# Performance work log

Hardware: AMD Instinct MI355X
Metric: run time of the kernel (lower is better)

Reference implementation:

```python
import jax, jax.numpy as jnp
import numpy as np

B, S, D, H = 2, 2048, 2048, 16
HD = D // H            # 128
HALF = HD // 2         # 64
SOFTCAP = 50.0
ROPE_BASE = 10000.0


def setup_inputs() -> dict:
    key = jax.random.key(0)
    k1, k2, k3 = jax.random.split(key, 3)
    inputs = jax.random.normal(k1, (B, S, D), dtype=jnp.float32)
    # param init ~ nnx.initializers.normal() (stddev 0.01 default; scale to keep activations sane)
    w_in = jax.random.normal(k2, (D, H, 3 * HD), dtype=jnp.float32) * (1.0 / np.sqrt(D))
    w_out = jax.random.normal(k3, (H, HD, D), dtype=jnp.float32) * (1.0 / np.sqrt(D))
    # RoPE tables: [S, HALF]
    pos = jnp.arange(S, dtype=jnp.float32)[:, None]
    inv_freq = 1.0 / (ROPE_BASE ** (jnp.arange(HALF, dtype=jnp.float32) / HALF))
    ang = pos * inv_freq[None, :]
    rope_sin = jnp.sin(ang)
    rope_cos = jnp.cos(ang)
    # causal mask [1, 1, S, S]
    mask = jnp.tril(jnp.ones((S, S), dtype=bool))[None, None, :, :]
    return {"inputs": inputs, "w_in": w_in, "w_out": w_out,
            "rope_sin": rope_sin, "rope_cos": rope_cos, "mask": mask}


def apply_rope(x, sin, cos):
    # x: [B, S, H, HD]; sin/cos: [S, HALF] -> broadcast [1, S, 1, HALF]
    sin = sin[None, :, None, :]
    cos = cos[None, :, None, :]
    x1, x2 = x[..., :HALF], x[..., HALF:]
    return jnp.concatenate([x1 * cos - x2 * sin, x2 * cos + x1 * sin], axis=-1)


def reference(inputs, w_in, w_out, rope_sin, rope_cos, mask):
    dtype = inputs.dtype
    # fused QKV projection: [B, S, H, 3*HD]
    qkv = jnp.einsum('bsd,bhf->bshf'.replace('bhf', 'dhf'), inputs, w_in)
    q, k, v = jnp.split(qkv, 3, axis=-1)           # each [B, S, H, HD]
    q = apply_rope(q, rope_sin, rope_cos)
    k = apply_rope(k, rope_sin, rope_cos)
    q = q / jnp.sqrt(jnp.asarray(HD, dtype))
    scores = jnp.einsum('bqhd,bkhd->bhqk', q, k)   # [B, H, S, S]
    big_neg = jnp.finfo(dtype).min
    scores = jnp.where(mask, scores, big_neg)
    scores = jnp.tanh(scores / SOFTCAP) * SOFTCAP  # softcap
    attn = jax.nn.softmax(scores, axis=-1)
    x = jnp.einsum('bhqk,bkhd->bqhd', attn, v)     # [B, S, H, HD]
    out = jnp.einsum('bqhd,hdm->bqm', x, w_out)    # [B, S, D]
    return out
```

## Files before the change

kernel.cpp:

```cpp
#include <hip/hip_runtime.h>

#define B_ 2
#define S_ 2048
#define D_ 2048
#define H_ 16
#define HD_ 128
#define NT_ (S_ / 64)
#define NBUF 6

typedef unsigned short u16;
typedef __bf16 bf16x8 __attribute__((ext_vector_type(8)));
typedef float f32x4 __attribute__((ext_vector_type(4)));

__device__ __forceinline__ float bf2f(u16 u) {
  unsigned int x = ((unsigned int)u) << 16;
  return __builtin_bit_cast(float, x);
}
__device__ __forceinline__ u16 f2bf(float f) {
  unsigned int u = __builtin_bit_cast(unsigned int, f);
  u += 0x7fffu + ((u >> 16) & 1u);
  return (u16)(u >> 16);
}
__device__ __forceinline__ void async16(const void* g, void* l) {
  __builtin_amdgcn_global_load_lds((const __attribute__((address_space(1))) void*)g,
                                   (__attribute__((address_space(3))) void*)l, 16, 0, 0);
}
__device__ __forceinline__ float vexp2(float x) {
  float r;
  asm("v_exp_f32 %0, %1" : "=v"(r) : "v"(x));
  return r;
}
__device__ __forceinline__ float vrcp(float x) {
  float r;
  asm("v_rcp_f32 %0, %1" : "=v"(r) : "v"(x));
  return r;
}

__global__ __launch_bounds__(256) void conv_f32_bf16(const float* __restrict__ in,
                                                     u16* __restrict__ outp, int n) {
  int idx = (blockIdx.x * 256 + threadIdx.x) * 4;
  int stride = gridDim.x * 256 * 4;
  for (; idx < n; idx += stride) {
    float4 v = *(const float4*)(in + idx);
    ushort4 ov = make_ushort4(f2bf(v.x), f2bf(v.y), f2bf(v.z), f2bf(v.w));
    *(ushort4*)(outp + idx) = ov;
  }
}

__global__ __launch_bounds__(256) void transpose_conv(const float* __restrict__ in,
                                                      u16* __restrict__ outp, int R, int C) {
  __shared__ float tile[32][33];
  int c0 = blockIdx.x * 32, r0 = blockIdx.y * 32;
  int tx = threadIdx.x & 31, ty = threadIdx.x >> 5;
#pragma unroll
  for (int yy = 0; yy < 32; yy += 8)
    tile[ty + yy][tx] = in[(size_t)(r0 + ty + yy) * C + c0 + tx];
  __syncthreads();
#pragma unroll
  for (int yy = 0; yy < 32; yy += 8)
    outp[(size_t)(c0 + ty + yy) * R + r0 + tx] = f2bf(tile[tx][ty + yy]);
}

__global__ __launch_bounds__(256) void transpose_v(const u16* __restrict__ in,
                                                   u16* __restrict__ outp) {
  __shared__ u16 tile[32][33];
  int bhh = blockIdx.z;
  const u16* ip = in + (size_t)bhh * S_ * HD_;
  u16* op = outp + (size_t)bhh * HD_ * S_;
  int hd0 = blockIdx.x * 32, s0 = blockIdx.y * 32;
  int tx = threadIdx.x & 31, ty = threadIdx.x >> 5;
#pragma unroll
  for (int yy = 0; yy < 32; yy += 8)
    tile[ty + yy][tx] = ip[(size_t)(s0 + ty + yy) * HD_ + hd0 + tx];
  __syncthreads();
#pragma unroll
  for (int yy = 0; yy < 32; yy += 8)
    op[(size_t)(hd0 + ty + yy) * S_ + s0 + tx] = tile[tx][ty + yy];
}

__global__ __launch_bounds__(256) void rope_kernel(u16* __restrict__ Q, u16* __restrict__ Kk,
                                                   const float* __restrict__ rsin,
                                                   const float* __restrict__ rcos) {
  int t = blockIdx.x * 256 + threadIdx.x;
  u16* base = blockIdx.y ? Kk : Q;
  float scale = blockIdx.y ? 1.0f : 0.08838834764831845f;
  int row = t >> 3, seg = t & 7;
  int s = row & (S_ - 1);
  int i0 = seg * 8;
  u16* p = base + (size_t)row * HD_;
  alignas(16) u16 x1[8], x2[8], o1[8], o2[8];
  *(uint4*)x1 = *(const uint4*)(p + i0);
  *(uint4*)x2 = *(const uint4*)(p + 64 + i0);
  alignas(16) float sn[8], cs[8];
  *(float4*)sn = *(const float4*)(rsin + s * 64 + i0);
  *(float4*)(sn + 4) = *(const float4*)(rsin + s * 64 + i0 + 4);
  *(float4*)cs = *(const float4*)(rcos + s * 64 + i0);
  *(float4*)(cs + 4) = *(const float4*)(rcos + s * 64 + i0 + 4);
#pragma unroll
  for (int j = 0; j < 8; ++j) {
    float a = bf2f(x1[j]), bb = bf2f(x2[j]);
    o1[j] = f2bf((a * cs[j] - bb * sn[j]) * scale);
    o2[j] = f2bf((bb * cs[j] + a * sn[j]) * scale);
  }
  *(uint4*)(p + i0) = *(uint4*)o1;
  *(uint4*)(p + 64 + i0) = *(uint4*)o2;
}

#define BAR __builtin_amdgcn_s_barrier()
#define LGKM0                                          \
  {                                                    \
    asm volatile("s_waitcnt lgkmcnt(0)" ::: "memory"); \
    __builtin_amdgcn_sched_barrier(0);                 \
  }
#define VM4 asm volatile("s_waitcnt vmcnt(4)" ::: "memory")
#define VM0 asm volatile("s_waitcnt vmcnt(0)" ::: "memory")
#define P1 __builtin_amdgcn_s_setprio(1)
#define P0 __builtin_amdgcn_s_setprio(0)

template <int EPI>
__global__ __launch_bounds__(512, 1) void gemm256_8p(const u16* __restrict__ A,
                                                     const u16* __restrict__ Bt,
                                                     float* __restrict__ C, int K, int N,
                                                     int ntn, u16* __restrict__ Qo,
                                                     u16* __restrict__ Ko, u16* __restrict__ Vo) {
  __shared__ alignas(16) u16 lsA[2][256 * 64];
  __shared__ alignas(16) u16 lsB[2][256 * 64];
  const int tid = threadIdx.x;
  const int lane = tid & 63, wid = tid >> 6;
  const int g = lane >> 4, lr = lane & 15;
  const int wm = wid >> 2, wn = wid & 3;

  const int nwg = 16 * ntn;
  const int bid = blockIdx.x;
  const int swz = (bid & 7) * (nwg >> 3) + (bid >> 3);
  const int m_idx = swz & 15, n_idx = swz >> 4;
  const size_t m0 = (size_t)m_idx * 256, n0 = (size_t)n_idx * 256;

  const int row0 = tid >> 3, sl0 = tid & 7;
  const int row1 = (512 + tid) >> 3, sl1 = tid & 7;
  const u16* pA0 = A + (m0 + row0) * K + ((sl0 ^ (row0 & 7)) << 3);
  const u16* pA1 = A + (m0 + row1) * K + ((sl1 ^ (row1 & 7)) << 3);
  const u16* pB0 = Bt + (n0 + row0) * K + ((sl0 ^ (row0 & 7)) << 3);
  const u16* pB1 = Bt + (n0 + row1) * K + ((sl1 ^ (row1 & 7)) << 3);
  const size_t hstep = (size_t)128 * K;

#define STG_A(t, buf, half)                                                                   \
  {                                                                                           \
    async16(pA0 + (half) * hstep + (size_t)(t) * 64, (char*)lsA[buf] + (half) * 16384 + tid * 16); \
    async16(pA1 + (half) * hstep + (size_t)(t) * 64,                                          \
            (char*)lsA[buf] + (half) * 16384 + 8192 + tid * 16);                              \
  }
#define STG_B(t, buf, half)                                                                   \
  {                                                                                           \
    async16(pB0 + (half) * hstep + (size_t)(t) * 64, (char*)lsB[buf] + (half) * 16384 + tid * 16); \
    async16(pB1 + (half) * hstep + (size_t)(t) * 64,                                          \
            (char*)lsB[buf] + (half) * 16384 + 8192 + tid * 16);                              \
  }

  const int sw0 = ((g) ^ (lr & 7)) << 4;
  const int sw1 = ((4 + g) ^ (lr & 7)) << 4;

#define LDA(tb, mh)                                                              \
  {                                                                              \
    _Pragma("unroll") for (int i2 = 0; i2 < 4; ++i2) {                           \
      const char* _p = (const char*)lsA[tb] + (wm * 128 + (mh)*64 + i2 * 16 + lr) * 128; \
      aF[i2][0] = *(const bf16x8*)(_p + sw0);                                    \
      aF[i2][1] = *(const bf16x8*)(_p + sw1);                                    \
    }                                                                            \
  }
#define LDB(tb, dst, nh)                                                         \
  {                                                                              \
    _Pragma("unroll") for (int j2 = 0; j2 < 2; ++j2) {                           \
      const char* _p = (const char*)lsB[tb] + (wn * 64 + (nh)*32 + j2 * 16 + lr) * 128; \
      dst[j2][0] = *(const bf16x8*)(_p + sw0);                                   \
      dst[j2][1] = *(const bf16x8*)(_p + sw1);                                   \
    }                                                                            \
  }
#define MM(mh, nh, BB)                                                                        \
  {                                                                                           \
    _Pragma("unroll") for (int i2 = 0; i2 < 4; ++i2) _Pragma("unroll") for (int j2 = 0;      \
                                                                            j2 < 2; ++j2) {  \
      acc[(mh)*4 + i2][(nh)*2 + j2] = __builtin_amdgcn_mfma_f32_16x16x32_bf16(                \
          aF[i2][0], BB[j2][0], acc[(mh)*4 + i2][(nh)*2 + j2], 0, 0, 0);                      \
      acc[(mh)*4 + i2][(nh)*2 + j2] = __builtin_amdgcn_mfma_f32_16x16x32_bf16(                \
          aF[i2][1], BB[j2][1], acc[(mh)*4 + i2][(nh)*2 + j2], 0, 0, 0);                      \
    }                                                                                         \
  }

  f32x4 acc[8][4] = {};
  const int nk2 = K >> 7;

  STG_A(0, 0, 0);
  STG_B(0, 0, 1);
  STG_B(0, 0, 0);
  STG_A(0, 0, 1);
  STG_A(1, 1, 0);
  STG_B(1, 1, 1);
  VM4;
  BAR;

  bf16x8 aF[4][2], b0[2][2], b1[2][2];
#pragma unroll 1
  for (int it = 0; it < nk2 - 1; ++it) {
    const int t1 = 2 * it + 1, s2 = 2 * it + 2, s3 = 2 * it + 3;
    LDA(0, 0);
    LDB(0, b0, 0);
    STG_B(t1, 1, 0);
    BAR; LGKM0; P1; MM(0, 0, b0); P0; BAR;
    LDB(0, b1, 1);
    STG_A(t1, 1, 1);
    BAR; LGKM0; P1; MM(0, 1, b1); P0; BAR;
    LDA(0, 1);
    STG_A(s2, 0, 0);
    BAR; LGKM0; P1; MM(1, 1, b1); P0; BAR;
    STG_B(s2, 0, 1);
    BAR; LGKM0; P1; MM(1, 0, b0); P0;
    VM4;
    BAR;
    LDA(1, 0);
    LDB(1, b0, 0);
    STG_B(s2, 0, 0);
    BAR; LGKM0; P1; MM(0, 0, b0); P0; BAR;
    LDB(1, b1, 1);
    STG_A(s2, 0, 1);
    BAR; LGKM0; P1; MM(0, 1, b1); P0; BAR;
    LDA(1, 1);
    STG_A(s3, 1, 0);
    BAR; LGKM0; P1; MM(1, 1, b1); P0; BAR;
    STG_B(s3, 1, 1);
    BAR; LGKM0; P1; MM(1, 0, b0); P0;
    VM4;
    BAR;
  }
  {
    const int t1 = 2 * (nk2 - 1) + 1;
    LDA(0, 0);
    LDB(0, b0, 0);
    STG_B(t1, 1, 0);
    BAR; LGKM0; P1; MM(0, 0, b0); P0; BAR;
    LDB(0, b1, 1);
    STG_A(t1, 1, 1);
    BAR; LGKM0; P1; MM(0, 1, b1); P0; BAR;
    LDA(0, 1);
    BAR; LGKM0; P1; MM(1, 1, b1); P0; BAR;
    BAR; LGKM0; P1; MM(1, 0, b0); P0;
    VM0;
    BAR;
    LDA(1, 0);
    LDB(1, b0, 0);
    BAR; LGKM0; P1; MM(0, 0, b0); P0; BAR;
    LDB(1, b1, 1);
    BAR; LGKM0; P1; MM(0, 1, b1); P0; BAR;
    LDA(1, 1);
    BAR; LGKM0; P1; MM(1, 1, b1); P0; BAR;
    BAR; LGKM0; P1; MM(1, 0, b0); P0; BAR;
  }
#undef STG_A
#undef STG_B
#undef LDA
#undef LDB
#undef MM

  if (EPI == 0) {
#pragma unroll
    for (int ai = 0; ai < 8; ++ai)
#pragma unroll
      for (int bj = 0; bj < 4; ++bj)
#pragma unroll
        for (int r = 0; r < 4; ++r) {
          size_t m = m0 + wm * 128 + (ai >> 2) * 64 + (ai & 3) * 16 + 4 * g + r;
          size_t n = n0 + wn * 64 + (bj >> 1) * 32 + (bj & 1) * 16 + lr;
          C[m * N + n] = acc[ai][bj][r];
        }
  } else {
    const int c = (int)(n0 >> 7) + (wn >> 1);
    const int h = c / 3, part = c % 3;
    u16* dst = (part == 0) ? Qo : (part == 1 ? Ko : Vo);
#pragma unroll
    for (int ai = 0; ai < 8; ++ai)
#pragma unroll
      for (int bj = 0; bj < 4; ++bj)
#pragma unroll
        for (int r = 0; r < 4; ++r) {
          int m = (int)m0 + wm * 128 + (ai >> 2) * 64 + (ai & 3) * 16 + 4 * g + r;
          int hd = (wn & 1) * 64 + (bj >> 1) * 32 + (bj & 1) * 16 + lr;
          int b = m >> 11, s = m & (S_ - 1);
          dst[((size_t)(b * H_ + h) * S_ + s) * HD_ + hd] = f2bf(acc[ai][bj][r]);
        }
  }
}

template <int EPI>
__global__ __launch_bounds__(512, 1) void gemm8p(const u16* __restrict__ A,
                                                 const u16* __restrict__ Bt,
                                                 float* __restrict__ C, int K, int N, int gx,
                                                 u16* __restrict__ Qo, u16* __restrict__ Ko,
                                                 u16* __restrict__ Vo) {
  __shared__ alignas(16) u16 lsA[NBUF][256 * 32];
  __shared__ alignas(16) u16 lsB[NBUF][128 * 32];
  const int tid = threadIdx.x;
  const int lane = tid & 63;
  const int wid = tid >> 6;
  const int g = lane >> 4, lr = lane & 15;
  const int wm = wid >> 1, wn = wid & 1;

  const int nwg = gx << 4;
  const int bid = blockIdx.x;
  const int swz = (bid & 7) * (nwg >> 3) + (bid >> 3);
  const int m_idx = swz & 15, n_idx = swz >> 4;
  const size_t m0 = (size_t)m_idx * 256, n0 = (size_t)n_idx * 128;

  const int la0 = tid, la1 = 512 + tid;
  const int rowA0 = la0 >> 2, slA0 = la0 & 3;
  const int rowA1 = la1 >> 2, slA1 = la1 & 3;
  const int rowB = tid >> 2, slB = tid & 3;
  const u16* srcA0 = A + (m0 + rowA0) * K + ((slA0 ^ ((rowA0 >> 1) & 3)) << 3);
  const u16* srcA1 = A + (m0 + rowA1) * K + ((slA1 ^ ((rowA1 >> 1) & 3)) << 3);
  const u16* srcB = Bt + (n0 + rowB) * K + ((slB ^ ((rowB >> 1) & 3)) << 3);

#define STAGE(t, bufi)                                  \
  {                                                     \
    const int koff = (t) << 5;                          \
    async16(srcA0 + koff, (char*)lsA[bufi] + la0 * 16); \
    async16(srcA1 + koff, (char*)lsA[bufi] + la1 * 16); \
    async16(srcB + koff, (char*)lsB[bufi] + tid * 16);  \
  }

  int ofsA[4], ofsB[4];
#pragma unroll
  for (int i = 0; i < 4; ++i) {
    int ra = wm * 64 + i * 16 + lr;
    ofsA[i] = ra * 64 + ((g ^ ((ra >> 1) & 3)) << 4);
    int rb = wn * 64 + i * 16 + lr;
    ofsB[i] = rb * 64 + ((g ^ ((rb >> 1) & 3)) << 4);
  }

  f32x4 acc[4][4] = {};
  const int nk = K >> 5;

#pragma unroll
  for (int t = 0; t < NBUF - 1; ++t) STAGE(t, t);
  asm volatile("s_waitcnt vmcnt(12)" ::: "memory");
  __builtin_amdgcn_s_barrier();

  int buf = 0;
#pragma unroll 1
  for (int kt = 0; kt < nk; ++kt) {
    bf16x8 af[4], bfr[4];
#pragma unroll
    for (int i = 0; i < 4; ++i) af[i] = *(const bf16x8*)((const char*)lsA[buf] + ofsA[i]);
#pragma unroll
    for (int j = 0; j < 4; ++j) bfr[j] = *(const bf16x8*)((const char*)lsB[buf] + ofsB[j]);
    const int st = kt + NBUF - 1;
    const int sbuf = buf == 0 ? NBUF - 1 : buf - 1;
    if (st < nk) STAGE(st, sbuf);
    __builtin_amdgcn_s_barrier();
    __builtin_amdgcn_s_setprio(1);
#pragma unroll
    for (int i = 0; i < 4; ++i)
#pragma unroll
      for (int j = 0; j < 4; ++j)
        acc[i][j] = __builtin_amdgcn_mfma_f32_16x16x32_bf16(af[i], bfr[j], acc[i][j], 0, 0, 0);
    __builtin_amdgcn_s_setprio(0);
    asm volatile("s_waitcnt vmcnt(12)" ::: "memory");
    __builtin_amdgcn_s_barrier();
    buf = buf == NBUF - 1 ? 0 : buf + 1;
  }
#undef STAGE

  if (EPI == 0) {
#pragma unroll
    for (int i = 0; i < 4; ++i)
#pragma unroll
      for (int j = 0; j < 4; ++j)
#pragma unroll
        for (int r = 0; r < 4; ++r) {
          size_t m = m0 + wm * 64 + i * 16 + 4 * g + r;
          size_t n = n0 + wn * 64 + j * 16 + lr;
          C[m * N + n] = acc[i][j][r];
        }
  } else {
    const int part = n_idx % 3, h = n_idx / 3;
    u16* dst = (part == 0) ? Qo : (part == 1 ? Ko : Vo);
#pragma unroll
    for (int i = 0; i < 4; ++i)
#pragma unroll
      for (int j = 0; j < 4; ++j)
#pragma unroll
        for (int r = 0; r < 4; ++r) {
          int m = (int)m0 + wm * 64 + i * 16 + 4 * g + r;
          int hd = wn * 64 + j * 16 + lr;
          int b = m >> 11, s = m & (S_ - 1);
          dst[((size_t)(b * H_ + h) * S_ + s) * HD_ + hd] = f2bf(acc[i][j][r]);
        }
  }
}

__global__ __launch_bounds__(256) void attn_fwd(const u16* __restrict__ Q, const u16* __restrict__ K,
                                                const u16* __restrict__ VT, u16* __restrict__ X) {
  const int bx = blockIdx.x;
  const int bh = blockIdx.y;
  const int tid = threadIdx.x;
  const int lane = tid & 63, wid = tid >> 6;
  const int g = lane >> 4, lr = lane & 15;

  __shared__ alignas(16) u16 lsK[2][64 * 128];
  __shared__ alignas(16) u16 lsV[2][128 * 64];
  __shared__ alignas(16) u16 lsP[4][16 * 72];

  const u16* Qp = Q + (size_t)bh * S_ * HD_;
  const u16* Kp = K + (size_t)bh * S_ * HD_;
  const u16* Vp = VT + (size_t)bh * HD_ * S_;
  u16* myP = lsP[wid];
  const int b = bh >> 4, h = bh & 15;

  const float c1 = -0.057707802f;
  const float c2 = -144.26950409f;

#pragma unroll 1
  for (int pass = 0; pass < 2; ++pass) {
    const int qt = pass ? bx : (NT_ - 1 - bx);
    const int qrow = qt * 64 + wid * 16 + lr;
    const int qbase = qt * 64 + wid * 16 + 4 * g;

    bf16x8 qf[4];
#pragma unroll
    for (int kc = 0; kc < 4; ++kc)
      qf[kc] = *(const bf16x8*)(Qp + (size_t)qrow * HD_ + kc * 32 + g * 8);

    f32x4 o[8] = {};
    float psum[4] = {0.f, 0.f, 0.f, 0.f};

#pragma unroll
    for (int p = 0; p < 4; ++p) {
      int c = p * 256 + tid;
      int rowk = c >> 4;
      int wsk = ((c & 15) << 4) ^ ((rowk & 7) << 4);
      async16((const char*)Kp + (((size_t)rowk) << 8) + wsk, (char*)lsK[0] + c * 16);
      int rowv = c >> 3;
      int wsv = ((c & 7) << 4) ^ ((rowv & 7) << 4);
      async16((const char*)Vp + (size_t)rowv * (S_ * 2) + wsv, (char*)lsV[0] + c * 16);
    }
    __syncthreads();

    int cur = 0;
    for (int kt = 0; kt <= qt; ++kt) {
      if (kt < qt) {
        const int nxt = kt + 1;
#pragma unroll
        for (int p = 0; p < 4; ++p) {
          int c = p * 256 + tid;
          int rowk = c >> 4;
          int wsk = ((c & 15) << 4) ^ ((rowk & 7) << 4);
          async16((const char*)Kp + (((size_t)(nxt * 64 + rowk)) << 8) + wsk,
                  (char*)lsK[cur ^ 1] + c * 16);
          int rowv = c >> 3;
          int wsv = ((c & 7) << 4) ^ ((rowv & 7) << 4);
          async16((const char*)Vp + (size_t)rowv * (S_ * 2) + nxt * 128 + wsv,
                  (char*)lsV[cur ^ 1] + c * 16);
        }
      }
      f32x4 sc[4];
#pragma unroll
      for (int jn = 0; jn < 4; ++jn) {
        f32x4 a = {0.f, 0.f, 0.f, 0.f};
        const int row = jn * 16 + lr;
        const int sw = (row & 7) << 4;
#pragma unroll
        for (int kc = 0; kc < 4; ++kc) {
          int w = (kc * 64 + g * 16) ^ sw;
          bf16x8 kf = *(const bf16x8*)((const char*)lsK[cur] + row * 256 + w);
          a = __builtin_amdgcn_mfma_f32_16x16x32_bf16(qf[kc], kf, a, 0, 0, 0);
        }
        sc[jn] = a;
      }
#pragma unroll
      for (int jn = 0; jn < 4; ++jn) {
        int key = kt * 64 + jn * 16 + lr;
#pragma unroll
        for (int r = 0; r < 4; ++r) {
          float z = vexp2(c1 * sc[jn][r]);
          float p = vexp2(c2 * z * vrcp(1.f + z));
          if (key > qbase + r) p = 0.f;
          psum[r] += p;
          myP[(4 * g + r) * 72 + jn * 16 + lr] = f2bf(p);
        }
      }
#pragma unroll
      for (int kc = 0; kc < 2; ++kc) {
        bf16x8 pa = *(const bf16x8*)(myP + lr * 72 + kc * 32 + g * 8);
#pragma unroll
        for (int jh = 0; jh < 8; ++jh) {
          int row = jh * 16 + lr;
          int w = (kc * 64 + g * 16) ^ ((row & 7) << 4);
          bf16x8 vf = *(const bf16x8*)((const char*)lsV[cur] + row * 128 + w);
          o[jh] = __builtin_amdgcn_mfma_f32_16x16x32_bf16(pa, vf, o[jh], 0, 0, 0);
        }
      }
      __syncthreads();
      cur ^= 1;
    }
    float lsum[4];
#pragma unroll
    for (int r = 0; r < 4; ++r) {
      float s = psum[r];
#pragma unroll
      for (int msk = 1; msk < 16; msk <<= 1) s += __shfl_xor(s, msk, 64);
      lsum[r] = s;
    }
#pragma unroll
    for (int r = 0; r < 4; ++r) {
      float inv = 1.f / lsum[r];
      int s = qbase + r;
      u16* xp = X + ((size_t)(b * S_ + s)) * D_ + h * HD_;
#pragma unroll
      for (int jh = 0; jh < 8; ++jh) xp[jh * 16 + lr] = f2bf(o[jh][r] * inv);
    }
  }
}

extern "C" void kernel_launch(void* const* d_in, const int* in_sizes, int n_in,
                              void* d_out, int out_size, void* d_ws, size_t ws_size,
                              hipStream_t stream) {
  const float* inputs = (const float*)d_in[0];
  const float* w_in = (const float*)d_in[1];
  const float* w_out = (const float*)d_in[2];
  const float* rsin = (const float*)d_in[3];
  const float* rcos = (const float*)d_in[4];
  float* out = (float*)d_out;

  char* ws = (char*)d_ws;
  u16* bfA = (u16*)(ws);
  u16* w_inT = (u16*)(ws + 16777216);
  u16* Qraw = (u16*)(ws + 41943040);
  u16* Kraw = (u16*)(ws + 58720256);
  u16* Vraw = (u16*)(ws + 75497472);
  u16* VT = (u16*)(ws + 92274688);
  u16* Xbuf = (u16*)(ws);
  u16* w_outT = (u16*)(ws + 16777216);

  conv_f32_bf16<<<2048, 256, 0, stream>>>(inputs, bfA, B_ * S_ * D_);
  transpose_conv<<<dim3(6144 / 32, 2048 / 32), 256, 0, stream>>>(w_in, w_inT, 2048, 6144);
  gemm256_8p<1><<<384, 512, 0, stream>>>(bfA, w_inT, nullptr, 2048, 6144, 24,
                                         Qraw, Kraw, Vraw);
  transpose_conv<<<dim3(2048 / 32, 2048 / 32), 256, 0, stream>>>(w_out, w_outT, 2048, 2048);
  rope_kernel<<<dim3(2048, 2), 256, 0, stream>>>(Qraw, Kraw, rsin, rcos);
  transpose_v<<<dim3(4, 64, 32), 256, 0, stream>>>(Vraw, VT);
  attn_fwd<<<dim3(NT_ / 2, 32), 256, 0, stream>>>(Qraw, Kraw, VT, Xbuf);
  gemm8p<0><<<256, 512, 0, stream>>>(Xbuf, w_outT, out, 2048, 2048, 16,
                                     nullptr, nullptr, nullptr);
}
```

Before: 294.8 us.

## Fuse RoPE and V transpose into QKV GEMM epilogue via permuted weight columns

The w_in transpose now permutes output columns so each wave holds matching RoPE pairs (d and d+64) in its accumulators. The QKV GEMM epilogue then applies RoPE and the Q scaling directly, and writes V already transposed. This removes the separate rope_kernel and transpose_v launches and their extra global memory round trips. In exchange the epilogue does extra sin/cos table loads and its stores are scattered, with V written as strided ushort4 stores.

```diff
diff --git a/kernel.cpp b/kernel.cpp
--- a/kernel.cpp
+++ b/kernel.cpp
@@ -61,49 +61,23 @@
     outp[(size_t)(c0 + ty + yy) * R + r0 + tx] = f2bf(tile[tx][ty + yy]);
 }
 
-__global__ __launch_bounds__(256) void transpose_v(const u16* __restrict__ in,
-                                                   u16* __restrict__ outp) {
-  __shared__ u16 tile[32][33];
-  int bhh = blockIdx.z;
-  const u16* ip = in + (size_t)bhh * S_ * HD_;
-  u16* op = outp + (size_t)bhh * HD_ * S_;
-  int hd0 = blockIdx.x * 32, s0 = blockIdx.y * 32;
+__global__ __launch_bounds__(256) void transpose_win(const float* __restrict__ in,
+                                                     u16* __restrict__ outp) {
+  __shared__ float tile[32][33];
+  int n0 = blockIdx.x * 32, k0 = blockIdx.y * 32;
   int tx = threadIdx.x & 31, ty = threadIdx.x >> 5;
+  int n = n0 + tx;
+  int cc = n >> 7, p = n & 127;
+  int q = (p >> 4) & 3;
+  int d = ((p >> 6) << 5) + ((q >> 1) << 4) + ((q & 1) << 6) + (p & 15);
+  int f = (cc / 3) * 384 + (cc % 3) * 128 + d;
 #pragma unroll
   for (int yy = 0; yy < 32; yy += 8)
-    tile[ty + yy][tx] = ip[(size_t)(s0 + ty + yy) * HD_ + hd0 + tx];
+    tile[ty + yy][tx] = in[(size_t)(k0 + ty + yy) * 6144 + f];
   __syncthreads();
 #pragma unroll
   for (int yy = 0; yy < 32; yy += 8)
-    op[(size_t)(hd0 + ty + yy) * S_ + s0 + tx] = tile[tx][ty + yy];
-}
-
-__global__ __launch_bounds__(256) void rope_kernel(u16* __restrict__ Q, u16* __restrict__ Kk,
-                                                   const float* __restrict__ rsin,
-                                                   const float* __restrict__ rcos) {
-  int t = blockIdx.x * 256 + threadIdx.x;
-  u16* base = blockIdx.y ? Kk : Q;
-  float scale = blockIdx.y ? 1.0f : 0.08838834764831845f;
-  int row = t >> 3, seg = t & 7;
-  int s = row & (S_ - 1);
-  int i0 = seg * 8;
-  u16* p = base + (size_t)row * HD_;
-  alignas(16) u16 x1[8], x2[8], o1[8], o2[8];
-  *(uint4*)x1 = *(const uint4*)(p + i0);
-  *(uint4*)x2 = *(const uint4*)(p + 64 + i0);
-  alignas(16) float sn[8], cs[8];
-  *(float4*)sn = *(const float4*)(rsin + s * 64 + i0);
-  *(float4*)(sn + 4) = *(const float4*)(rsin + s * 64 + i0 + 4);
-  *(float4*)cs = *(const float4*)(rcos + s * 64 + i0);
-  *(float4*)(cs + 4) = *(const float4*)(rcos + s * 64 + i0 + 4);
-#pragma unroll
-  for (int j = 0; j < 8; ++j) {
-    float a = bf2f(x1[j]), bb = bf2f(x2[j]);
-    o1[j] = f2bf((a * cs[j] - bb * sn[j]) * scale);
-    o2[j] = f2bf((bb * cs[j] + a * sn[j]) * scale);
-  }
-  *(uint4*)(p + i0) = *(uint4*)o1;
-  *(uint4*)(p + 64 + i0) = *(uint4*)o2;
+    outp[(size_t)(n0 + ty + yy) * 2048 + k0 + tx] = f2bf(tile[tx][ty + yy]);
 }
 
 #define BAR __builtin_amdgcn_s_barrier()
@@ -118,11 +92,10 @@
 #define P0 __builtin_amdgcn_s_setprio(0)
 
 template <int EPI>
-__global__ __launch_bounds__(512, 1) void gemm256_8p(const u16* __restrict__ A,
-                                                     const u16* __restrict__ Bt,
-                                                     float* __restrict__ C, int K, int N,
-                                                     int ntn, u16* __restrict__ Qo,
-                                                     u16* __restrict__ Ko, u16* __restrict__ Vo) {
+__global__ __launch_bounds__(512, 1) void gemm256_8p(
+    const u16* __restrict__ A, const u16* __restrict__ Bt, float* __restrict__ C, int K, int N,
+    int ntn, u16* __restrict__ Qo, u16* __restrict__ Ko, u16* __restrict__ Vo,
+    const float* __restrict__ rsin, const float* __restrict__ rcos) {
   __shared__ alignas(16) u16 lsA[2][256 * 64];
   __shared__ alignas(16) u16 lsB[2][256 * 64];
   const int tid = threadIdx.x;
@@ -144,47 +117,45 @@
   const u16* pB1 = Bt + (n0 + row1) * K + ((sl1 ^ (row1 & 7)) << 3);
   const size_t hstep = (size_t)128 * K;
 
-#define STG_A(t, buf, half)                                                                   \
-  {                                                                                           \
-    async16(pA0 + (half) * hstep + (size_t)(t) * 64, (char*)lsA[buf] + (half) * 16384 + tid * 16); \
-    async16(pA1 + (half) * hstep + (size_t)(t) * 64,                                          \
-            (char*)lsA[buf] + (half) * 16384 + 8192 + tid * 16);                              \
-  }
-#define STG_B(t, buf, half)                                                                   \
-  {                                                                                           \
-    async16(pB0 + (half) * hstep + (size_t)(t) * 64, (char*)lsB[buf] + (half) * 16384 + tid * 16); \
-    async16(pB1 + (half) * hstep + (size_t)(t) * 64,                                          \
-            (char*)lsB[buf] + (half) * 16384 + 8192 + tid * 16);                              \
+#define STG_A(t, buf, half)                                                                        \
+  {                                                                                                \
+    async16(pA0 + (half)*hstep + (size_t)(t)*64, (char*)lsA[buf] + (half)*16384 + tid * 16);       \
+    async16(pA1 + (half)*hstep + (size_t)(t)*64, (char*)lsA[buf] + (half)*16384 + 8192 + tid * 16); \
+  }
+#define STG_B(t, buf, half)                                                                        \
+  {                                                                                                \
+    async16(pB0 + (half)*hstep + (size_t)(t)*64, (char*)lsB[buf] + (half)*16384 + tid * 16);       \
+    async16(pB1 + (half)*hstep + (size_t)(t)*64, (char*)lsB[buf] + (half)*16384 + 8192 + tid * 16); \
   }
 
   const int sw0 = ((g) ^ (lr & 7)) << 4;
   const int sw1 = ((4 + g) ^ (lr & 7)) << 4;
 
-#define LDA(tb, mh)                                                              \
-  {                                                                              \
-    _Pragma("unroll") for (int i2 = 0; i2 < 4; ++i2) {                           \
+#define LDA(tb, mh)                                                                      \
+  {                                                                                      \
+    _Pragma("unroll") for (int i2 = 0; i2 < 4; ++i2) {                                   \
       const char* _p = (const char*)lsA[tb] + (wm * 128 + (mh)*64 + i2 * 16 + lr) * 128; \
-      aF[i2][0] = *(const bf16x8*)(_p + sw0);                                    \
-      aF[i2][1] = *(const bf16x8*)(_p + sw1);                                    \
-    }                                                                            \
-  }
-#define LDB(tb, dst, nh)                                                         \
-  {                                                                              \
-    _Pragma("unroll") for (int j2 = 0; j2 < 2; ++j2) {                           \
+      aF[i2][0] = *(const bf16x8*)(_p + sw0);                                            \
+      aF[i2][1] = *(const bf16x8*)(_p + sw1);                                            \
+    }                                                                                    \
+  }
+#define LDB(tb, dst, nh)                                                                \
+  {                                                                                     \
+    _Pragma("unroll") for (int j2 = 0; j2 < 2; ++j2) {                                  \
       const char* _p = (const char*)lsB[tb] + (wn * 64 + (nh)*32 + j2 * 16 + lr) * 128; \
-      dst[j2][0] = *(const bf16x8*)(_p + sw0);                                   \
-      dst[j2][1] = *(const bf16x8*)(_p + sw1);                                   \
-    }                                                                            \
-  }
-#define MM(mh, nh, BB)                                                                        \
-  {                                                                                           \
-    _Pragma("unroll") for (int i2 = 0; i2 < 4; ++i2) _Pragma("unroll") for (int j2 = 0;      \
-                                                                            j2 < 2; ++j2) {  \
-      acc[(mh)*4 + i2][(nh)*2 + j2] = __builtin_amdgcn_mfma_f32_16x16x32_bf16(                \
-          aF[i2][0], BB[j2][0], acc[(mh)*4 + i2][(nh)*2 + j2], 0, 0, 0);                      \
-      acc[(mh)*4 + i2][(nh)*2 + j2] = __builtin_amdgcn_mfma_f32_16x16x32_bf16(                \
-          aF[i2][1], BB[j2][1], acc[(mh)*4 + i2][(nh)*2 + j2], 0, 0, 0);                      \
-    }                                                                                         \
+      dst[j2][0] = *(const bf16x8*)(_p + sw0);                                          \
+      dst[j2][1] = *(const bf16x8*)(_p + sw1);                                          \
+    }                                                                                   \
+  }
+#define MM(mh, nh, BB)                                                                       \
+  {                                                                                          \
+    _Pragma("unroll") for (int i2 = 0; i2 < 4; ++i2) _Pragma("unroll") for (int j2 = 0;     \
+                                                                            j2 < 2; ++j2) { \
+      acc[(mh)*4 + i2][(nh)*2 + j2] = __builtin_amdgcn_mfma_f32_16x16x32_bf16(               \
+          aF[i2][0], BB[j2][0], acc[(mh)*4 + i2][(nh)*2 + j2], 0, 0, 0);                     \
+      acc[(mh)*4 + i2][(nh)*2 + j2] = __builtin_amdgcn_mfma_f32_16x16x32_bf16(               \
+          aF[i2][1], BB[j2][1], acc[(mh)*4 + i2][(nh)*2 + j2], 0, 0, 0);                     \
+    }                                                                                        \
   }
 
   f32x4 acc[8][4] = {};
@@ -275,18 +246,47 @@
   } else {
     const int c = (int)(n0 >> 7) + (wn >> 1);
     const int h = c / 3, part = c % 3;
-    u16* dst = (part == 0) ? Qo : (part == 1 ? Ko : Vo);
-#pragma unroll
-    for (int ai = 0; ai < 8; ++ai)
-#pragma unroll
-      for (int bj = 0; bj < 4; ++bj)
+    const int wn1 = wn & 1;
+    if (part == 2) {
+#pragma unroll
+      for (int ai = 0; ai < 8; ++ai) {
+        int m = (int)m0 + wm * 128 + (ai >> 2) * 64 + (ai & 3) * 16 + 4 * g;
+        int b = m >> 11, s = m & (S_ - 1);
+#pragma unroll
+        for (int bj = 0; bj < 4; ++bj) {
+          int hd = wn1 * 32 + ((bj >> 1) << 4) + ((bj & 1) << 6) + lr;
+          ushort4 pk;
+          pk.x = f2bf(acc[ai][bj][0]);
+          pk.y = f2bf(acc[ai][bj][1]);
+          pk.z = f2bf(acc[ai][bj][2]);
+          pk.w = f2bf(acc[ai][bj][3]);
+          *(ushort4*)(Vo + ((size_t)(b * H_ + h) * HD_ + hd) * S_ + s) = pk;
+        }
+      }
+    } else {
+      u16* dstp = (part == 0) ? Qo : Ko;
+      const float scl = (part == 0) ? 0.08838834764831845f : 1.0f;
+#pragma unroll
+      for (int ai = 0; ai < 8; ++ai) {
+        int mbase = (int)m0 + wm * 128 + (ai >> 2) * 64 + (ai & 3) * 16 + 4 * g;
 #pragma unroll
         for (int r = 0; r < 4; ++r) {
-          int m = (int)m0 + wm * 128 + (ai >> 2) * 64 + (ai & 3) * 16 + 4 * g + r;
-          int hd = (wn & 1) * 64 + (bj >> 1) * 32 + (bj & 1) * 16 + lr;
+          int m = mbase + r;
           int b = m >> 11, s = m & (S_ - 1);
-          dst[((size_t)(b * H_ + h) * S_ + s) * HD_ + hd] = f2bf(acc[ai][bj][r]);
-        }
+          const float* srow = rsin + s * 64;
+          const float* crow = rcos + s * 64;
+          u16* op = dstp + ((size_t)(b * H_ + h) * S_ + s) * HD_;
+#pragma unroll
+          for (int t = 0; t < 2; ++t) {
+            int d = wn1 * 32 + t * 16 + lr;
+            float cv = crow[d] * scl, sv = srow[d] * scl;
+            float x1 = acc[ai][t * 2][r], x2 = acc[ai][t * 2 + 1][r];
+            op[d] = f2bf(x1 * cv - x2 * sv);
+            op[d + 64] = f2bf(x2 * cv + x1 * sv);
+          }
+        }
+      }
+    }
   }
 }
 
@@ -534,18 +534,15 @@
   u16* w_inT = (u16*)(ws + 16777216);
   u16* Qraw = (u16*)(ws + 41943040);
   u16* Kraw = (u16*)(ws + 58720256);
-  u16* Vraw = (u16*)(ws + 75497472);
-  u16* VT = (u16*)(ws + 92274688);
+  u16* VT = (u16*)(ws + 75497472);
   u16* Xbuf = (u16*)(ws);
   u16* w_outT = (u16*)(ws + 16777216);
 
   conv_f32_bf16<<<2048, 256, 0, stream>>>(inputs, bfA, B_ * S_ * D_);
-  transpose_conv<<<dim3(6144 / 32, 2048 / 32), 256, 0, stream>>>(w_in, w_inT, 2048, 6144);
-  gemm256_8p<1><<<384, 512, 0, stream>>>(bfA, w_inT, nullptr, 2048, 6144, 24,
-                                         Qraw, Kraw, Vraw);
-  transpose_conv<<<dim3(2048 / 32, 2048 / 32), 256, 0, stream>>>(w_out, w_outT, 2048, 2048);
-  rope_kernel<<<dim3(2048, 2), 256, 0, stream>>>(Qraw, Kraw, rsin, rcos);
-  transpose_v<<<dim3(4, 64, 32), 256, 0, stream>>>(Vraw, VT);
+  transpose_win<<<dim3(192, 64), 256, 0, stream>>>(w_in, w_inT);
+  gemm256_8p<1><<<384, 512, 0, stream>>>(bfA, w_inT, nullptr, 2048, 6144, 24, Qraw, Kraw, VT,
+                                         rsin, rcos);
+  transpose_conv<<<dim3(64, 64), 256, 0, stream>>>(w_out, w_outT, 2048, 2048);
   attn_fwd<<<dim3(NT_ / 2, 32), 256, 0, stream>>>(Qraw, Kraw, VT, Xbuf);
   gemm8p<0><<<256, 512, 0, stream>>>(Xbuf, w_outT, out, 2048, 2048, 16,
                                      nullptr, nullptr, nullptr);
```

Result: faster. 288.3 us (-2.2%).
